# Performance work log

Hardware: AMD Instinct MI355X
Metric: run time of the kernel (lower is better)

## Reference

```python
import jax, jax.numpy as jnp
import numpy as np

B, N, M, D, H = 4, 512, 4096, 256, 8
HD = D // H


def setup_inputs() -> dict:
    key = jax.random.key(0)
    ks = jax.random.split(key, 10)
    s = 1.0 / np.sqrt(D)
    return {
        "amr_feats": jax.random.normal(ks[0], (B, N, D), jnp.float32),
        "amr_pad_mask": jax.random.randint(ks[1], (B, N), 0, 2) == 1,
        "visual_feats": jax.random.normal(ks[2], (B, M, D), jnp.float32),
        "W_amr_qk": jax.random.normal(ks[3], (D, D), jnp.float32) * s,
        "W_amr_v": jax.random.normal(ks[4], (D, D), jnp.float32) * s,
        "W_vis_qk": jax.random.normal(ks[5], (D, D), jnp.float32) * s,
        "W_vis_v": jax.random.normal(ks[6], (D, D), jnp.float32) * s,
        "W_amr_out": jax.random.normal(ks[7], (D, D), jnp.float32) * s,
        "b_amr_out": jnp.zeros((D,), jnp.float32),
        "W_vis_out": jax.random.normal(ks[8], (D, D), jnp.float32) * s,
        "b_vis_out": jnp.zeros((D,), jnp.float32),
    }


def _split_heads(x):  # [b, s, d] -> [b, h, s, hd]
    b, s, _ = x.shape
    return x.reshape(b, s, H, HD).transpose(0, 2, 1, 3)


def _merge_heads(x):  # [b, h, s, hd] -> [b, s, d]
    b, _, s, _ = x.shape
    return x.transpose(0, 2, 1, 3).reshape(b, s, H * HD)


def reference(amr_feats, amr_pad_mask, visual_feats,
              W_amr_qk, W_amr_v, W_vis_qk, W_vis_v,
              W_amr_out, b_amr_out, W_vis_out, b_vis_out):
    scale = HD ** -0.5
    amr_qk = _split_heads(amr_feats @ W_amr_qk)      # [b,h,n,hd]
    vis_qk = _split_heads(visual_feats @ W_vis_qk)   # [b,h,m,hd]
    amr_v = _split_heads(amr_feats @ W_amr_v)        # [b,h,n,hd]
    vis_v = _split_heads(visual_feats @ W_vis_v)     # [b,h,m,hd]

    # shared score matrix, computed once and reused for both directions
    common = jnp.einsum('bhnc,bhmc->bhnm', amr_qk, vis_qk) * scale  # [b,h,n,m]

    # amr -> visual (visual_pads is None in the top-level forward: no mask)
    amr_vis_w = jax.nn.softmax(common, axis=-1)
    amr_feats_2 = _merge_heads(jnp.einsum('bhnm,bhmc->bhnc', amr_vis_w, vis_v))
    amr_feats_2 = amr_feats_2 @ W_amr_out + b_amr_out

    # visual -> amr, masked by amr_pad_mask
    neg = jnp.finfo(common.dtype).min
    vis_txt = jnp.where(amr_pad_mask[:, None, None, :], neg,
                        common.transpose(0, 1, 3, 2))  # [b,h,m,n]
    vis_txt_w = jax.nn.softmax(vis_txt, axis=-1)
    visual_feats_2 = _merge_heads(jnp.einsum('bhmn,bhnc->bhmc', vis_txt_w, amr_v))
    visual_feats_2 = visual_feats_2 @ W_vis_out + b_vis_out

    # text_trans == 'dot', visual_trans == 'dot'
    return amr_feats_2 * amr_feats, visual_feats * visual_feats_2
```

## Files before the change

kernel.cpp:

```cpp
#include <hip/hip_runtime.h>

#define BB 4
#define NN 512
#define MM 4096
#define DD 256
#define HH 8
#define HDD 32

typedef __attribute__((ext_vector_type(8))) short bf16x8;
typedef __attribute__((ext_vector_type(4))) float f32x4;
typedef __attribute__((ext_vector_type(4))) unsigned int u32x4;

__device__ __forceinline__ unsigned short f2b(float f) {
    union { float f; unsigned u; } v; v.f = f;
    unsigned r = v.u + 0x7fffu + ((v.u >> 16) & 1u);
    return (unsigned short)(r >> 16);
}
__device__ __forceinline__ float b2f(unsigned short u) {
    union { unsigned u; float f; } v; v.u = ((unsigned)u) << 16;
    return v.f;
}
__device__ __forceinline__ unsigned cvt_pk_bf16(float lo, float hi) {
    unsigned r;
    asm("v_cvt_pk_bf16_f32 %0, %1, %2" : "=v"(r) : "v"(lo), "v"(hi));
    return r;
}

struct WPack { const float* s[6]; unsigned short* d[6]; };
__global__ __launch_bounds__(256) void convert_w(WPack p)
{
    __shared__ unsigned short T[64][72];
    const int mat = blockIdx.x >> 4;
    const int tile = blockIdx.x & 15;
    const int kt = (tile >> 2) * 64, ct = (tile & 3) * 64;
    const int t = threadIdx.x;
    const int kl = t >> 2, cseg = (t & 3) * 16;

    const float* src = &p.s[mat][(size_t)(kt + kl) * DD + ct + cseg];
    #pragma unroll
    for (int j4 = 0; j4 < 4; ++j4) {
        const float4 f = *(const float4*)(src + j4 * 4);
        T[cseg + j4 * 4 + 0][kl] = f2b(f.x);
        T[cseg + j4 * 4 + 1][kl] = f2b(f.y);
        T[cseg + j4 * 4 + 2][kl] = f2b(f.z);
        T[cseg + j4 * 4 + 3][kl] = f2b(f.w);
    }
    __syncthreads();
    unsigned short* dst = &p.d[mat][(size_t)(ct + kl) * DD + kt + cseg];
    *(bf16x8*)dst       = *(const bf16x8*)&T[kl][cseg];
    *(bf16x8*)(dst + 8) = *(const bf16x8*)&T[kl][cseg + 8];
}

template<int OUTMODE>
__device__ __forceinline__ void gemm_tile_in(
    const float* __restrict__ A,
    const unsigned short* __restrict__ Wt,
    float outscale,
    unsigned short* __restrict__ Cb,
    unsigned short* __restrict__ VT, int SEQ,
    int r0, int c0,
    unsigned short (*As)[72], unsigned short (*Ws)[72])
{
    const int tid = threadIdx.x;
    const int lane = tid & 63, w = tid >> 6;
    const int rq = (w >> 1) * 32, cq = (w & 1) * 32;
    const int srow = tid >> 2, skc = (tid & 3) * 16;
    const int g = lane >> 4, cl = lane & 15;

    f32x4 acc[2][2] = {};

    for (int ks = 0; ks < DD; ks += 64) {
        __syncthreads();
        {
            const float* ga = &A[(size_t)(r0 + srow) * DD + ks + skc];
            const float4 f0 = *(const float4*)(ga);
            const float4 f1 = *(const float4*)(ga + 4);
            const float4 f2 = *(const float4*)(ga + 8);
            const float4 f3 = *(const float4*)(ga + 12);
            uint4 u0, u1;
            u0.x = cvt_pk_bf16(f0.x, f0.y); u0.y = cvt_pk_bf16(f0.z, f0.w);
            u0.z = cvt_pk_bf16(f1.x, f1.y); u0.w = cvt_pk_bf16(f1.z, f1.w);
            u1.x = cvt_pk_bf16(f2.x, f2.y); u1.y = cvt_pk_bf16(f2.z, f2.w);
            u1.z = cvt_pk_bf16(f3.x, f3.y); u1.w = cvt_pk_bf16(f3.z, f3.w);
            *(uint4*)&As[srow][skc]     = u0;
            *(uint4*)&As[srow][skc + 8] = u1;
            const unsigned short* gw = &Wt[(size_t)(c0 + srow) * DD + ks + skc];
            *(bf16x8*)&Ws[srow][skc]     = *(const bf16x8*)gw;
            *(bf16x8*)&Ws[srow][skc + 8] = *(const bf16x8*)(gw + 8);
        }
        __syncthreads();
        #pragma unroll
        for (int kh = 0; kh < 2; ++kh) {
            const int kk = kh * 32 + g * 8;
            const bf16x8 a0 = *(const bf16x8*)&As[rq + cl][kk];
            const bf16x8 a1 = *(const bf16x8*)&As[rq + 16 + cl][kk];
            const bf16x8 b0 = *(const bf16x8*)&Ws[cq + cl][kk];
            const bf16x8 b1 = *(const bf16x8*)&Ws[cq + 16 + cl][kk];
            acc[0][0] = __builtin_amdgcn_mfma_f32_16x16x32_bf16(a0, b0, acc[0][0], 0, 0, 0);
            acc[0][1] = __builtin_amdgcn_mfma_f32_16x16x32_bf16(a0, b1, acc[0][1], 0, 0, 0);
            acc[1][0] = __builtin_amdgcn_mfma_f32_16x16x32_bf16(a1, b0, acc[1][0], 0, 0, 0);
            acc[1][1] = __builtin_amdgcn_mfma_f32_16x16x32_bf16(a1, b1, acc[1][1], 0, 0, 0);
        }
    }

    if (OUTMODE == 0) {
        #pragma unroll
        for (int sr = 0; sr < 2; ++sr)
        #pragma unroll
        for (int sc = 0; sc < 2; ++sc) {
            const int col = c0 + cq + sc * 16 + cl;
            #pragma unroll
            for (int reg = 0; reg < 4; ++reg) {
                const int row = r0 + rq + sr * 16 + g * 4 + reg;
                Cb[(size_t)row * DD + col] = f2b(acc[sr][sc][reg] * outscale);
            }
        }
    } else {
        __syncthreads();
        #pragma unroll
        for (int sr = 0; sr < 2; ++sr)
        #pragma unroll
        for (int sc = 0; sc < 2; ++sc) {
            const int col_local = cq + sc * 16 + cl;
            uint2 u;
            u.x = cvt_pk_bf16(acc[sr][sc][0], acc[sr][sc][1]);
            u.y = cvt_pk_bf16(acc[sr][sc][2], acc[sr][sc][3]);
            *(uint2*)&As[col_local][rq + g * 8 + sr * 4] = u;
        }
        __syncthreads();
        const int col = tid >> 2, seg = tid & 3;
        const int b = r0 / SEQ, m0 = r0 % SEQ;
        unsigned short* dst = &VT[((size_t)b * DD + c0 + col) * SEQ + m0 + seg * 16];
        *(bf16x8*)dst       = *(const bf16x8*)&As[col][seg * 16];
        *(bf16x8*)(dst + 8) = *(const bf16x8*)&As[col][seg * 16 + 8];
    }
}

struct InPack {
    const float* amr; const float* vis;
    const unsigned short *Wqa, *Wva, *Wqv, *Wvv;
    unsigned short *amr_qk, *vis_qk, *VTa, *VTv;
    float sqs;
};
__global__ __launch_bounds__(256) void gemm_in(InPack p)
{
    __shared__ unsigned short As[64][72];
    __shared__ unsigned short Ws[64][72];
    const int bx = blockIdx.x;
    const int c0 = blockIdx.y * 64;
    if (bx < 32)
        gemm_tile_in<0>(p.amr, p.Wqa, p.sqs, p.amr_qk, nullptr, 0, bx * 64, c0, As, Ws);
    else if (bx < 64)
        gemm_tile_in<2>(p.amr, p.Wva, 1.f, nullptr, p.VTa, NN, (bx - 32) * 64, c0, As, Ws);
    else if (bx < 320)
        gemm_tile_in<0>(p.vis, p.Wqv, p.sqs, p.vis_qk, nullptr, 0, (bx - 64) * 64, c0, As, Ws);
    else
        gemm_tile_in<2>(p.vis, p.Wvv, 1.f, nullptr, p.VTv, MM, (bx - 320) * 64, c0, As, Ws);
}

__device__ __forceinline__ void gemm_tile_out(
    const unsigned short* __restrict__ A,
    const unsigned short* __restrict__ Wt,
    const float* __restrict__ bias,
    const float* __restrict__ feats,
    float* __restrict__ Cf,
    int r0, int c0,
    unsigned short (*As)[72], unsigned short (*Ws)[72])
{
    const int tid = threadIdx.x;
    const int lane = tid & 63, w = tid >> 6;
    const int rq = (w >> 1) * 32, cq = (w & 1) * 32;
    const int srow = tid >> 2, skc = (tid & 3) * 16;
    const int g = lane >> 4, cl = lane & 15;

    f32x4 acc[2][2] = {};

    for (int ks = 0; ks < DD; ks += 64) {
        __syncthreads();
        {
            const unsigned short* ga = &A[(size_t)(r0 + srow) * DD + ks + skc];
            *(bf16x8*)&As[srow][skc]     = *(const bf16x8*)ga;
            *(bf16x8*)&As[srow][skc + 8] = *(const bf16x8*)(ga + 8);
            const unsigned short* gw = &Wt[(size_t)(c0 + srow) * DD + ks + skc];
            *(bf16x8*)&Ws[srow][skc]     = *(const bf16x8*)gw;
            *(bf16x8*)&Ws[srow][skc + 8] = *(const bf16x8*)(gw + 8);
        }
        __syncthreads();
        #pragma unroll
        for (int kh = 0; kh < 2; ++kh) {
            const int kk = kh * 32 + g * 8;
            const bf16x8 a0 = *(const bf16x8*)&As[rq + cl][kk];
            const bf16x8 a1 = *(const bf16x8*)&As[rq + 16 + cl][kk];
            const bf16x8 b0 = *(const bf16x8*)&Ws[cq + cl][kk];
            const bf16x8 b1 = *(const bf16x8*)&Ws[cq + 16 + cl][kk];
            acc[0][0] = __builtin_amdgcn_mfma_f32_16x16x32_bf16(a0, b0, acc[0][0], 0, 0, 0);
            acc[0][1] = __builtin_amdgcn_mfma_f32_16x16x32_bf16(a0, b1, acc[0][1], 0, 0, 0);
            acc[1][0] = __builtin_amdgcn_mfma_f32_16x16x32_bf16(a1, b0, acc[1][0], 0, 0, 0);
            acc[1][1] = __builtin_amdgcn_mfma_f32_16x16x32_bf16(a1, b1, acc[1][1], 0, 0, 0);
        }
    }

    #pragma unroll
    for (int sr = 0; sr < 2; ++sr)
    #pragma unroll
    for (int sc = 0; sc < 2; ++sc) {
        const int col = c0 + cq + sc * 16 + cl;
        #pragma unroll
        for (int reg = 0; reg < 4; ++reg) {
            const int row = r0 + rq + sr * 16 + g * 4 + reg;
            const size_t idx = (size_t)row * DD + col;
            Cf[idx] = (acc[sr][sc][reg] + bias[col]) * feats[idx];
        }
    }
}

struct OutPack {
    const unsigned short* A[2];
    const unsigned short* Wt[2];
    const float* bias[2];
    const float* feats[2];
    float* O[2];
};
__global__ __launch_bounds__(256) void gemm_out(OutPack p)
{
    __shared__ unsigned short As[64][72];
    __shared__ unsigned short Ws[64][72];
    const int bx = blockIdx.x;
    const int which = (bx < 32) ? 0 : 1;
    const int rb = (bx < 32) ? bx : bx - 32;
    gemm_tile_out(p.A[which], p.Wt[which], p.bias[which], p.feats[which],
                  p.O[which], rb * 64, blockIdx.y * 64, As, Ws);
}

template<int SEQK, int SPLIT, bool HAS_MASK>
__device__ __forceinline__ void attn_body(
    int bid,
    const unsigned short* __restrict__ Qb,
    const unsigned short* __restrict__ Kb,
    const unsigned short* __restrict__ VTb,
    const int* __restrict__ mask,
    unsigned short* __restrict__ ctx,
    float* __restrict__ Pl, unsigned short* __restrict__ PaccB,
    int NQ, float* maskadd)
{
    constexpr int KCHUNK = SEQK / SPLIT;
    constexpr int NT = KCHUNK / 64;

    const int tid = threadIdx.x;
    const int lane = tid & 63, w = tid >> 6;
    const int g = lane >> 4, cl = lane & 15;

    const int nqt = NQ / 256;
    int bi = bid;
    const int sp = bi % SPLIT; bi /= SPLIT;
    const int qt = bi % nqt;   bi /= nqt;
    const int h  = bi % HH;
    const int b  = bi / HH;
    const int q0 = qt * 256 + w * 64;
    const int kv0 = sp * KCHUNK;

    if (HAS_MASK) {
        for (int i = tid; i < SEQK; i += 256)
            maskadd[i] = mask[b * SEQK + i] ? -1e30f : 0.f;
        __syncthreads();
    }

    bf16x8 aq[4];
    #pragma unroll
    for (int qg = 0; qg < 4; ++qg)
        aq[qg] = *(const bf16x8*)
            &Qb[((size_t)b * NQ + q0 + qg * 16 + cl) * DD + h * HDD + g * 8];

    const unsigned short* Kp0 = Kb + (size_t)b * SEQK * DD + h * HDD + g * 8
                                   + (size_t)(kv0 + cl) * DD;
    const unsigned short* Vp0 = VTb + ((size_t)b * DD + h * HDD + cl) * SEQK
                                    + kv0 + g * 8;

    float lsum[4] = {0.f, 0.f, 0.f, 0.f};
    f32x4 acc[4][2] = {};

    bf16x8 Kc[4], Kn[4];
    #pragma unroll
    for (int kf = 0; kf < 4; ++kf)
        Kc[kf] = *(const bf16x8*)(Kp0 + (size_t)(kf * 16) * DD);

    for (int t = 0; t < NT; ++t) {
        const int m0 = kv0 + t * 64;

        if (t + 1 < NT) {
            const unsigned short* kp = Kp0 + (size_t)((t + 1) * 64) * DD;
            #pragma unroll
            for (int kf = 0; kf < 4; ++kf)
                Kn[kf] = *(const bf16x8*)(kp + (size_t)(kf * 16) * DD);
        }

        bf16x8 vv[2][2];
        #pragma unroll
        for (int mh = 0; mh < 2; ++mh)
            #pragma unroll
            for (int sub = 0; sub < 2; ++sub)
                vv[mh][sub] = *(const bf16x8*)
                    (Vp0 + (size_t)(sub * 16) * SEQK + t * 64 + mh * 32);

        uint2 X[4][4];
        #pragma unroll
        for (int kh = 0; kh < 2; ++kh) {
            f32x4 s[4][2];
            #pragma unroll
            for (int k2 = 0; k2 < 2; ++k2) {
                const f32x4 z = {0.f, 0.f, 0.f, 0.f};
                const bf16x8 kfrag = Kc[kh * 2 + k2];
                #pragma unroll
                for (int qg = 0; qg < 4; ++qg)
                    s[qg][k2] = __builtin_amdgcn_mfma_f32_16x16x32_bf16(
                        kfrag, aq[qg], z, 0, 0, 0);
            }
            #pragma unroll
            for (int k2 = 0; k2 < 2; ++k2) {
                const int kf = kh * 2 + k2;
                f32x4 madd;
                if (HAS_MASK)
                    madd = *(const f32x4*)&maskadd[m0 + kf * 16 + g * 4];
                #pragma unroll
                for (int qg = 0; qg < 4; ++qg) {
                    const float p0 = exp2f(s[qg][k2][0] + (HAS_MASK ? madd[0] : 0.f));
                    const float p1 = exp2f(s[qg][k2][1] + (HAS_MASK ? madd[1] : 0.f));
                    const float p2 = exp2f(s[qg][k2][2] + (HAS_MASK ? madd[2] : 0.f));
                    const float p3 = exp2f(s[qg][k2][3] + (HAS_MASK ? madd[3] : 0.f));
                    lsum[qg] += (p0 + p1) + (p2 + p3);
                    X[qg][kf].x = cvt_pk_bf16(p0, p1);
                    X[qg][kf].y = cvt_pk_bf16(p2, p3);
                }
            }
        }

        #pragma unroll
        for (int mh = 0; mh < 2; ++mh) {
            union { u32x4 u; bf16x8 b; } pa[4];
            #pragma unroll
            for (int qg = 0; qg < 4; ++qg) {
                pa[qg].u[0] = X[qg][mh * 2].x;
                pa[qg].u[1] = X[qg][mh * 2].y;
                pa[qg].u[2] = X[qg][mh * 2 + 1].x;
                pa[qg].u[3] = X[qg][mh * 2 + 1].y;
            }
            #pragma unroll
            for (int sub = 0; sub < 2; ++sub)
                #pragma unroll
                for (int qg = 0; qg < 4; ++qg)
                    acc[qg][sub] = __builtin_amdgcn_mfma_f32_16x16x32_bf16(
                        pa[qg].b, vv[mh][sub], acc[qg][sub], 0, 0, 0);
        }

        #pragma unroll
        for (int kf = 0; kf < 4; ++kf) Kc[kf] = Kn[kf];
    }

    #pragma unroll
    for (int qg = 0; qg < 4; ++qg) {
        lsum[qg] += __shfl_xor(lsum[qg], 16);
        lsum[qg] += __shfl_xor(lsum[qg], 32);
    }

    if (SPLIT > 1) {
        const int pb = bid;
        #pragma unroll
        for (int qg = 0; qg < 4; ++qg) {
            #pragma unroll
            for (int sub = 0; sub < 2; ++sub)
                #pragma unroll
                for (int reg = 0; reg < 4; ++reg) {
                    const int wq = w * 64 + qg * 16 + g * 4 + reg;
                    PaccB[((size_t)pb * 256 + wq) * 32 + sub * 16 + cl]
                        = f2b(acc[qg][sub][reg]);
                }
            if (g == 0)
                Pl[(size_t)pb * 256 + w * 64 + qg * 16 + cl] = lsum[qg];
        }
    } else {
        float linv[4][4];
        #pragma unroll
        for (int qg = 0; qg < 4; ++qg)
            #pragma unroll
            for (int reg = 0; reg < 4; ++reg)
                linv[qg][reg] = __shfl(lsum[qg], g * 4 + reg);
        #pragma unroll
        for (int qg = 0; qg < 4; ++qg)
            #pragma unroll
            for (int sub = 0; sub < 2; ++sub)
                #pragma unroll
                for (int reg = 0; reg < 4; ++reg) {
                    const int q = q0 + qg * 16 + g * 4 + reg;
                    ctx[((size_t)b * NQ + q) * DD + h * HDD + sub * 16 + cl]
                        = f2b(acc[qg][sub][reg] / linv[qg][reg]);
                }
    }
}

__global__ __launch_bounds__(256) void attn_fused(
    const unsigned short* __restrict__ amr_qk,
    const unsigned short* __restrict__ vis_qk,
    const unsigned short* __restrict__ VT_vis,
    const unsigned short* __restrict__ VT_amr,
    const int* __restrict__ mask,
    unsigned short* __restrict__ ctx1,
    float* __restrict__ Pl, unsigned short* __restrict__ PaccB)
{
    __shared__ float maskadd[NN];
    const int group = blockIdx.x / 3, rem = blockIdx.x % 3;
    if (rem < 2) {
        attn_body<MM, 16, false>(group * 2 + rem, amr_qk, vis_qk, VT_vis, nullptr,
                                 nullptr, Pl, PaccB, NN, maskadd);
    } else {
        attn_body<NN, 1, true>(group, vis_qk, amr_qk, VT_amr, mask,
                               ctx1, nullptr, nullptr, MM, maskadd);
    }
}

__global__ __launch_bounds__(256) void combine_split(
    const float* __restrict__ Pl, const unsigned short* __restrict__ PaccB,
    unsigned short* __restrict__ ctx)
{
    const int q = threadIdx.x;
    const int bqt = blockIdx.x;
    const int qt = bqt & 1, h = (bqt >> 1) & 7, b = bqt >> 4;
    const int pb0 = bqt * 16;

    float denom = 0.f;
    float o[32] = {};
    #pragma unroll
    for (int sp = 0; sp < 16; ++sp) {
        const size_t base = ((size_t)(pb0 + sp) * 256 + q) * 32;
        #pragma unroll
        for (int c8 = 0; c8 < 4; ++c8) {
            const bf16x8 a = *(const bf16x8*)&PaccB[base + c8 * 8];
            #pragma unroll
            for (int j = 0; j < 8; ++j)
                o[c8 * 8 + j] += b2f((unsigned short)a[j]);
        }
        denom += Pl[(size_t)(pb0 + sp) * 256 + q];
    }
    const float inv = 1.f / denom;

    unsigned short* dst = &ctx[((size_t)b * NN + qt * 256 + q) * DD + h * HDD];
    #pragma unroll
    for (int j4 = 0; j4 < 8; ++j4) {
        ushort4 u;
        u.x = f2b(o[j4 * 4 + 0] * inv); u.y = f2b(o[j4 * 4 + 1] * inv);
        u.z = f2b(o[j4 * 4 + 2] * inv); u.w = f2b(o[j4 * 4 + 3] * inv);
        *(ushort4*)(dst + j4 * 4) = u;
    }
}

extern "C" void kernel_launch(void* const* d_in, const int* in_sizes, int n_in,
                              void* d_out, int out_size, void* d_ws, size_t ws_size,
                              hipStream_t stream)
{
    const float* amr_feats    = (const float*)d_in[0];
    const int*   amr_pad_mask = (const int*)d_in[1];
    const float* visual_feats = (const float*)d_in[2];
    const float* W_amr_qk     = (const float*)d_in[3];
    const float* W_amr_v      = (const float*)d_in[4];
    const float* W_vis_qk     = (const float*)d_in[5];
    const float* W_vis_v      = (const float*)d_in[6];
    const float* W_amr_out    = (const float*)d_in[7];
    const float* b_amr_out    = (const float*)d_in[8];
    const float* W_vis_out    = (const float*)d_in[9];
    const float* b_vis_out    = (const float*)d_in[10];

    unsigned short* ws = (unsigned short*)d_ws;
    unsigned short* Wt_amr_qk  = ws;
    unsigned short* Wt_amr_v   = ws + 65536;
    unsigned short* Wt_vis_qk  = ws + 131072;
    unsigned short* Wt_vis_v   = ws + 196608;
    unsigned short* Wt_amr_out = ws + 262144;
    unsigned short* Wt_vis_out = ws + 327680;
    unsigned short* amr_qk_b   = ws + 393216;
    unsigned short* VT_amr     = ws + 917504;
    unsigned short* vis_qk_b   = ws + 1441792;
    unsigned short* VT_vis     = ws + 5636096;
    unsigned short* ctx0_b     = ws + 9830400;
    unsigned short* ctx1_b     = ws + 10354688;
    float* Pl                  = (float*)(ws + 14548992);
    unsigned short* PaccB      = ws + 15073280;

    float* out0 = (float*)d_out;
    float* out1 = out0 + (size_t)BB * NN * DD;

    const float SQS = 0.50500976f;

    WPack wp;
    wp.s[0] = W_amr_qk;  wp.d[0] = Wt_amr_qk;
    wp.s[1] = W_amr_v;   wp.d[1] = Wt_amr_v;
    wp.s[2] = W_vis_qk;  wp.d[2] = Wt_vis_qk;
    wp.s[3] = W_vis_v;   wp.d[3] = Wt_vis_v;
    wp.s[4] = W_amr_out; wp.d[4] = Wt_amr_out;
    wp.s[5] = W_vis_out; wp.d[5] = Wt_vis_out;
    convert_w<<<96, 256, 0, stream>>>(wp);

    InPack ip;
    ip.amr = amr_feats; ip.vis = visual_feats;
    ip.Wqa = Wt_amr_qk; ip.Wva = Wt_amr_v;
    ip.Wqv = Wt_vis_qk; ip.Wvv = Wt_vis_v;
    ip.amr_qk = amr_qk_b; ip.vis_qk = vis_qk_b;
    ip.VTa = VT_amr; ip.VTv = VT_vis;
    ip.sqs = SQS;
    gemm_in<<<dim3(576, 4), 256, 0, stream>>>(ip);

    attn_fused<<<1536, 256, 0, stream>>>(
        amr_qk_b, vis_qk_b, VT_vis, VT_amr, amr_pad_mask, ctx1_b, Pl, PaccB);
    combine_split<<<64, 256, 0, stream>>>(Pl, PaccB, ctx0_b);

    OutPack op;
    op.A[0] = ctx0_b; op.Wt[0] = Wt_amr_out; op.bias[0] = b_amr_out;
    op.feats[0] = amr_feats;    op.O[0] = out0;
    op.A[1] = ctx1_b; op.Wt[1] = Wt_vis_out; op.bias[1] = b_vis_out;
    op.feats[1] = visual_feats; op.O[1] = out1;
    gemm_out<<<dim3(288, 4), 256, 0, stream>>>(op);
}
```

Before: 108.2 us.

## Store Q/K projections head-major and halve split-K for amr attention

The QK projection outputs are now written as [b, h, seq, 32] instead of [b, seq, 256], so each head's K and Q rows become contiguous 64-byte rows rather than strided slices of a 512-byte row. The attention loads are updated to that layout. Separately, the amr→visual attention split over the KV axis drops from 16 chunks to 8, which halves the partial results combine_split has to reduce. The grid becomes 1024 blocks interleaving the two directions one-to-one. The head-major write uses scattered 2-byte stores, and each amr block now does more serial KV work with less parallelism.

```diff
diff --git a/kernel.cpp b/kernel.cpp
--- a/kernel.cpp
+++ b/kernel.cpp
@@ -104,15 +104,18 @@
     }
 
     if (OUTMODE == 0) {
+        const int b0 = r0 / SEQ, mbase = r0 % SEQ;
         #pragma unroll
         for (int sr = 0; sr < 2; ++sr)
         #pragma unroll
         for (int sc = 0; sc < 2; ++sc) {
             const int col = c0 + cq + sc * 16 + cl;
+            const int head = col >> 5, c32 = col & 31;
             #pragma unroll
             for (int reg = 0; reg < 4; ++reg) {
-                const int row = r0 + rq + sr * 16 + g * 4 + reg;
-                Cb[(size_t)row * DD + col] = f2b(acc[sr][sc][reg] * outscale);
+                const int m = mbase + rq + sr * 16 + g * 4 + reg;
+                Cb[(((size_t)b0 * HH + head) * SEQ + m) * 32 + c32]
+                    = f2b(acc[sr][sc][reg] * outscale);
             }
         }
     } else {
@@ -149,11 +152,11 @@
     const int bx = blockIdx.x;
     const int c0 = blockIdx.y * 64;
     if (bx < 32)
-        gemm_tile_in<0>(p.amr, p.Wqa, p.sqs, p.amr_qk, nullptr, 0, bx * 64, c0, As, Ws);
+        gemm_tile_in<0>(p.amr, p.Wqa, p.sqs, p.amr_qk, nullptr, NN, bx * 64, c0, As, Ws);
     else if (bx < 64)
         gemm_tile_in<2>(p.amr, p.Wva, 1.f, nullptr, p.VTa, NN, (bx - 32) * 64, c0, As, Ws);
     else if (bx < 320)
-        gemm_tile_in<0>(p.vis, p.Wqv, p.sqs, p.vis_qk, nullptr, 0, (bx - 64) * 64, c0, As, Ws);
+        gemm_tile_in<0>(p.vis, p.Wqv, p.sqs, p.vis_qk, nullptr, MM, (bx - 64) * 64, c0, As, Ws);
     else
         gemm_tile_in<2>(p.vis, p.Wvv, 1.f, nullptr, p.VTv, MM, (bx - 320) * 64, c0, As, Ws);
 }
@@ -269,12 +272,10 @@
     #pragma unroll
     for (int qg = 0; qg < 4; ++qg)
         aq[qg] = *(const bf16x8*)
-            &Qb[((size_t)b * NQ + q0 + qg * 16 + cl) * DD + h * HDD + g * 8];
-
-    const unsigned short* Kp0 = Kb + (size_t)b * SEQK * DD + h * HDD + g * 8
-                                   + (size_t)(kv0 + cl) * DD;
-    const unsigned short* Vp0 = VTb + ((size_t)b * DD + h * HDD + cl) * SEQK
-                                    + kv0 + g * 8;
+            &Qb[(((size_t)b * HH + h) * NQ + q0 + qg * 16 + cl) * 32 + g * 8];
+
+    const unsigned short* Kp0 = Kb + (((size_t)b * HH + h) * SEQK + kv0 + cl) * 32 + g * 8;
+    const unsigned short* Vp0 = VTb + ((size_t)b * DD + h * HDD + cl) * SEQK + kv0 + g * 8;
 
     float lsum[4] = {0.f, 0.f, 0.f, 0.f};
     f32x4 acc[4][2] = {};
@@ -282,16 +283,16 @@
     bf16x8 Kc[4], Kn[4];
     #pragma unroll
     for (int kf = 0; kf < 4; ++kf)
-        Kc[kf] = *(const bf16x8*)(Kp0 + (size_t)(kf * 16) * DD);
+        Kc[kf] = *(const bf16x8*)(Kp0 + (size_t)(kf * 16) * 32);
 
     for (int t = 0; t < NT; ++t) {
         const int m0 = kv0 + t * 64;
 
         if (t + 1 < NT) {
-            const unsigned short* kp = Kp0 + (size_t)((t + 1) * 64) * DD;
+            const unsigned short* kp = Kp0 + (size_t)((t + 1) * 64) * 32;
             #pragma unroll
             for (int kf = 0; kf < 4; ++kf)
-                Kn[kf] = *(const bf16x8*)(kp + (size_t)(kf * 16) * DD);
+                Kn[kf] = *(const bf16x8*)(kp + (size_t)(kf * 16) * 32);
         }
 
         bf16x8 vv[2][2];
@@ -407,12 +408,11 @@
     float* __restrict__ Pl, unsigned short* __restrict__ PaccB)
 {
     __shared__ float maskadd[NN];
-    const int group = blockIdx.x / 3, rem = blockIdx.x % 3;
-    if (rem < 2) {
-        attn_body<MM, 16, false>(group * 2 + rem, amr_qk, vis_qk, VT_vis, nullptr,
-                                 nullptr, Pl, PaccB, NN, maskadd);
+    if ((blockIdx.x & 1) == 0) {
+        attn_body<MM, 8, false>(blockIdx.x >> 1, amr_qk, vis_qk, VT_vis, nullptr,
+                                nullptr, Pl, PaccB, NN, maskadd);
     } else {
-        attn_body<NN, 1, true>(group, vis_qk, amr_qk, VT_amr, mask,
+        attn_body<NN, 1, true>(blockIdx.x >> 1, vis_qk, amr_qk, VT_amr, mask,
                                ctx1, nullptr, nullptr, MM, maskadd);
     }
 }
@@ -424,12 +424,12 @@
     const int q = threadIdx.x;
     const int bqt = blockIdx.x;
     const int qt = bqt & 1, h = (bqt >> 1) & 7, b = bqt >> 4;
-    const int pb0 = bqt * 16;
+    const int pb0 = bqt * 8;
 
     float denom = 0.f;
     float o[32] = {};
     #pragma unroll
-    for (int sp = 0; sp < 16; ++sp) {
+    for (int sp = 0; sp < 8; ++sp) {
         const size_t base = ((size_t)(pb0 + sp) * 256 + q) * 32;
         #pragma unroll
         for (int c8 = 0; c8 < 4; ++c8) {
@@ -507,7 +507,7 @@
     ip.sqs = SQS;
     gemm_in<<<dim3(576, 4), 256, 0, stream>>>(ip);
 
-    attn_fused<<<1536, 256, 0, stream>>>(
+    attn_fused<<<1024, 256, 0, stream>>>(
         amr_qk_b, vis_qk_b, VT_vis, VT_amr, amr_pad_mask, ctx1_b, Pl, PaccB);
     combine_split<<<64, 256, 0, stream>>>(Pl, PaccB, ctx0_b);
 
```

After: 94.35 us. -12.8%, faster.
